# Performance work log

Hardware: AMD Instinct MI355X
Metric: run time of the kernel (lower is better)

## Reference

```python
import jax, jax.numpy as jnp
import numpy as np

H = 64      # num query heads
HKV = 8     # num key/value heads
D = 64      # head_dim
HID = 2880  # hidden_size
B = 8       # batch (num sequences)
Q = 16      # query tokens per sequence
P = 128     # kv pages per sequence
PAGE = 16   # kv page size
NPAGES = 2048  # total pages in cache pool
NEG = -1e9  # finite stand-in for -inf mask (avoids inf arithmetic; exp underflows to 0 identically)


def setup_inputs() -> dict:
    key = jax.random.key(0)
    ks = jax.random.split(key, 6)
    n = B * Q
    S = P * PAGE
    hidden_states = jax.random.normal(ks[0], (n, HID), jnp.float32) * 0.02
    kv_cache_at_layer = jax.random.normal(ks[1], (NPAGES, 2, PAGE, HKV, D), jnp.float32)
    qkv_dim = D * (H + 2 * HKV)
    w_qkv = jax.random.normal(ks[2], (qkv_dim, HID), jnp.float32) * 0.02
    b_qkv = jnp.zeros((qkv_dim,), jnp.float32)
    w_o = jax.random.normal(ks[3], (HID, H * D), jnp.float32) * 0.02
    b_o = jnp.zeros((HID,), jnp.float32)
    sinks = jax.random.normal(ks[4], (H,), jnp.float32)
    qo_indptr = (jnp.arange(B + 1) * Q).astype(jnp.int32)
    kv_page_indptr = (jnp.arange(B + 1) * P).astype(jnp.int32)
    kv_last_page_lens = jnp.full((B,), PAGE, jnp.int32)
    kv_page_indices = jnp.asarray(np.random.default_rng(0).permutation(NPAGES)[:B * P], jnp.int32)
    # causal mask: query i of each sequence sits at absolute position S - Q + i
    qpos = S - Q + jnp.arange(Q)
    mask = jnp.where(jnp.arange(S)[None, :] <= qpos[:, None], 0.0, NEG).astype(jnp.float32)
    attention_mask = jnp.broadcast_to(mask[None], (B, Q, S)).reshape(-1)
    return dict(hidden_states=hidden_states, kv_cache_at_layer=kv_cache_at_layer,
                attention_mask=attention_mask, w_qkv=w_qkv, b_qkv=b_qkv, w_o=w_o, b_o=b_o,
                sinks=sinks, qo_indptr=qo_indptr, kv_page_indptr=kv_page_indptr,
                kv_last_page_lens=kv_last_page_lens, kv_page_indices=kv_page_indices)


def reference(hidden_states, kv_cache_at_layer, attention_mask, w_qkv, b_qkv, w_o, b_o,
              sinks, qo_indptr, kv_page_indptr, kv_last_page_lens, kv_page_indices):
    n = hidden_states.shape[0]
    b = qo_indptr.shape[0] - 1
    q_len = n // b                              # uniform ragged layout (see setup)
    p = kv_page_indices.shape[0] // b
    page = kv_cache_at_layer.shape[2]
    s = p * page
    g = H // HKV                                # query heads per kv head (GQA groups)
    scaling = D ** -0.5

    qkv = hidden_states @ w_qkv.T + b_qkv                       # [n, (H+2*HKV)*D]
    q = qkv[:, :H * D].reshape(b, q_len, HKV, g, D) * scaling    # [b q hkv g d]

    pages = kv_page_indices.reshape(b, p)
    k = kv_cache_at_layer[pages, 0].reshape(b, s, HKV, D)        # gather pages -> [b s hkv d]
    v = kv_cache_at_layer[pages, 1].reshape(b, s, HKV, D)

    scores = jnp.einsum('bqhgd,bshd->bhgqs', q, k).astype(jnp.float32)
    mask = attention_mask.reshape(b, q_len, s)
    # keys beyond the valid portion of the last page are invalid
    valid = jnp.arange(s)[None, :] < ((p - 1) * page + kv_last_page_lens[:, None])
    mask = jnp.where(valid[:, None, :], mask, NEG)
    scores = scores + mask[:, None, None, :, :]

    # online-softmax merge across pages is equivalent to this single pass;
    # running max starts at 0 in the original, hence the clamp to 0
    m = jnp.maximum(scores.max(axis=-1), 0.0)                    # [b hkv g q]
    pexp = jnp.exp(scores - m[..., None])                        # [b hkv g q s]
    sink = sinks.reshape(HKV, g).astype(jnp.float32)
    sum_exp = pexp.sum(axis=-1) + jnp.exp(sink[None, :, :, None] - m)
    num = jnp.einsum('bhgqs,bshd->bhgqd', pexp, v.astype(jnp.float32))
    attn = num / sum_exp[..., None]                              # [b hkv g q d]
    attn = attn.transpose(0, 3, 1, 2, 4).reshape(n, H * D)       # q (h d)
    return attn.astype(hidden_states.dtype) @ w_o.T + b_o
```

## Files before the change

### kernel.cpp

```cpp
#include <hip/hip_runtime.h>
#include <hip/hip_bf16.h>

#define BB      8
#define QL      16
#define NHKV    8
#define NG      8
#define DD      64
#define HIDN    2880
#define PP      128
#define PGSZ    16
#define SS      2048
#define NQ      4096
#define NSPLIT  8
#define KSQ     5
#define KCQ     576
#define KSO     8
#define KCO     512

typedef short bf16x8 __attribute__((ext_vector_type(8)));
typedef short short4v __attribute__((ext_vector_type(4)));
typedef float f32x4  __attribute__((ext_vector_type(4)));

__device__ inline short f2bf(float f) {
  __hip_bfloat16 h = __float2bfloat16(f);
  union { __hip_bfloat16 h; short s; } u; u.h = h;
  return u.s;
}

__device__ inline float bf2f(short s) {
  union { float f; unsigned u; } u;
  u.u = ((unsigned)(unsigned short)s) << 16;
  return u.f;
}

__device__ inline bf16x8 cvt8(float4 a, float4 b) {
  bf16x8 r;
  r[0] = f2bf(a.x); r[1] = f2bf(a.y); r[2] = f2bf(a.z); r[3] = f2bf(a.w);
  r[4] = f2bf(b.x); r[5] = f2bf(b.y); r[6] = f2bf(b.z); r[7] = f2bf(b.w);
  return r;
}

__device__ inline bf16x8 pack8(const float* __restrict__ p) {
  float4 a = *(const float4*)p;
  float4 b = *(const float4*)(p + 4);
  return cvt8(a, b);
}

__global__ __launch_bounds__(256) void k_qkv_split(const float* __restrict__ hid,
                                                   const float* __restrict__ wq,
                                                   short* __restrict__ qpart) {
  const int n0 = blockIdx.x * 32;
  const int ks = blockIdx.y;
  const int tid = threadIdx.x;
  const int wid = tid >> 6, lane = tid & 63;
  const int lo = lane & 15, hi = lane >> 4;
  const int m0 = wid * 32;

  const float* xr0 = hid + (size_t)(m0 + lo) * HIDN;
  const float* xr1 = hid + (size_t)(m0 + 16 + lo) * HIDN;
  const float* wr0 = wq + (size_t)(n0 + lo) * HIDN;
  const float* wr1 = wq + (size_t)(n0 + 16 + lo) * HIDN;
  const int kb = ks * KCQ + hi * 8;

  f32x4 acc[2][2];
#pragma unroll
  for (int mt = 0; mt < 2; ++mt)
#pragma unroll
    for (int nt = 0; nt < 2; ++nt) acc[mt][nt] = (f32x4){0.f, 0.f, 0.f, 0.f};

  float4 bufA[4][2], bufB[4][2];
#define LOADQ(dst, kk) { \
    dst[0][0] = *(const float4*)(xr0 + (kk)); dst[0][1] = *(const float4*)(xr0 + (kk) + 4); \
    dst[1][0] = *(const float4*)(xr1 + (kk)); dst[1][1] = *(const float4*)(xr1 + (kk) + 4); \
    dst[2][0] = *(const float4*)(wr0 + (kk)); dst[2][1] = *(const float4*)(wr0 + (kk) + 4); \
    dst[3][0] = *(const float4*)(wr1 + (kk)); dst[3][1] = *(const float4*)(wr1 + (kk) + 4); }
#define MFMAQ(buf) { \
    bf16x8 a0 = cvt8(buf[0][0], buf[0][1]); \
    bf16x8 a1 = cvt8(buf[1][0], buf[1][1]); \
    bf16x8 w0 = cvt8(buf[2][0], buf[2][1]); \
    bf16x8 w1 = cvt8(buf[3][0], buf[3][1]); \
    acc[0][0] = __builtin_amdgcn_mfma_f32_16x16x32_bf16(a0, w0, acc[0][0], 0, 0, 0); \
    acc[0][1] = __builtin_amdgcn_mfma_f32_16x16x32_bf16(a0, w1, acc[0][1], 0, 0, 0); \
    acc[1][0] = __builtin_amdgcn_mfma_f32_16x16x32_bf16(a1, w0, acc[1][0], 0, 0, 0); \
    acc[1][1] = __builtin_amdgcn_mfma_f32_16x16x32_bf16(a1, w1, acc[1][1], 0, 0, 0); }

  LOADQ(bufA, kb);
#pragma unroll
  for (int it = 0; it < 9; ++it) {
    const int kk = kb + it * 64;
    LOADQ(bufB, kk + 32);
    MFMAQ(bufA);
    if (it < 8) LOADQ(bufA, kk + 64);
    MFMAQ(bufB);
  }
#undef LOADQ
#undef MFMAQ

  short* qp = qpart + (size_t)ks * 128 * NQ;
#pragma unroll
  for (int mt = 0; mt < 2; ++mt)
#pragma unroll
    for (int nt = 0; nt < 2; ++nt)
#pragma unroll
      for (int r = 0; r < 4; ++r) {
        int m = m0 + mt * 16 + hi * 4 + r;
        int n = n0 + nt * 16 + lo;
        qp[(size_t)m * NQ + n] = f2bf(acc[mt][nt][r]);
      }
}

__global__ __launch_bounds__(256) void k_attn(const float* __restrict__ kvc,
                                              const int* __restrict__ pidx,
                                              const int* __restrict__ llen,
                                              const short* __restrict__ qpart,
                                              const float* __restrict__ bq,
                                              short* __restrict__ opart,
                                              float* __restrict__ lbuf) {
  const int blk = blockIdx.x;
  const int pair = blk >> 3, split = blk & 7;
  const int b = pair >> 3, kvh = pair & 7;
  const int tid = threadIdx.x;
  const int wid = tid >> 6, lane = tid & 63;
  const int lo = lane & 15, hi = lane >> 4;
  const int wrow = wid * 32;

  __shared__ short plds[128][72];
  __shared__ float vlds[64][65];

  bf16x8 qf[2][2];
#pragma unroll
  for (int mt = 0; mt < 2; ++mt) {
    int r = wrow + mt * 16 + lo;
    int g = r >> 4, qq = r & 15;
    int m = b * QL + qq;
    int h = kvh * NG + g;
#pragma unroll
    for (int kg = 0; kg < 2; ++kg) {
      int n = h * DD + kg * 32 + hi * 8;
      float4 bb0 = *(const float4*)(bq + n);
      float4 bb1 = *(const float4*)(bq + n + 4);
      float s[8];
      s[0] = bb0.x; s[1] = bb0.y; s[2] = bb0.z; s[3] = bb0.w;
      s[4] = bb1.x; s[5] = bb1.y; s[6] = bb1.z; s[7] = bb1.w;
#pragma unroll
      for (int k2 = 0; k2 < KSQ; ++k2) {
        bf16x8 p = *(const bf16x8*)(qpart + ((size_t)k2 * 128 + m) * NQ + n);
#pragma unroll
        for (int j = 0; j < 8; ++j) s[j] += bf2f(p[j]);
      }
      bf16x8 q8;
#pragma unroll
      for (int j = 0; j < 8; ++j) q8[j] = f2bf(s[j] * 0.125f);
      qf[mt][kg] = q8;
    }
  }

  float l_part[2][4];
  f32x4 o_acc[2][4];
#pragma unroll
  for (int mt = 0; mt < 2; ++mt)
#pragma unroll
    for (int j = 0; j < 4; ++j) l_part[mt][j] = 0.f;
#pragma unroll
  for (int mt = 0; mt < 2; ++mt)
#pragma unroll
    for (int dt = 0; dt < 4; ++dt) o_acc[mt][dt] = (f32x4){0.f, 0.f, 0.f, 0.f};

  const int sKeepEnd = (PP - 1) * PGSZ + llen[b];
  const int* pib = pidx + b * PP;
  const int sBeg = split * (SS / NSPLIT);
  const int sEnd = sBeg + (SS / NSPLIT);

  for (int s0 = sBeg; s0 < sEnd; s0 += 64) {
    const int p0 = s0 >> 4;

    float4 vreg[4];
    const int vsr = tid >> 4;
    const int vc4 = (tid & 15) * 4;
#pragma unroll
    for (int pc = 0; pc < 4; ++pc) {
      int pg = pib[p0 + pc];
      vreg[pc] = *(const float4*)(kvc +
          ((((size_t)pg * 2 + 1) * PGSZ + vsr) * NHKV + kvh) * DD + vc4);
    }

    f32x4 sc[2][4];
#pragma unroll
    for (int mt = 0; mt < 2; ++mt)
#pragma unroll
      for (int nt = 0; nt < 4; ++nt) sc[mt][nt] = (f32x4){0.f, 0.f, 0.f, 0.f};

#pragma unroll
    for (int nt = 0; nt < 4; ++nt) {
      int pg = pib[p0 + nt];
      const float* kp = kvc + ((((size_t)pg * 2 + 0) * PGSZ + lo) * NHKV + kvh) * DD;
#pragma unroll
      for (int kg = 0; kg < 2; ++kg) {
        bf16x8 kf = pack8(kp + kg * 32 + hi * 8);
        sc[0][nt] = __builtin_amdgcn_mfma_f32_16x16x32_bf16(qf[0][kg], kf, sc[0][nt], 0, 0, 0);
        sc[1][nt] = __builtin_amdgcn_mfma_f32_16x16x32_bf16(qf[1][kg], kf, sc[1][nt], 0, 0, 0);
      }
    }

    if (s0 + 64 > SS - QL) {
#pragma unroll
      for (int mt = 0; mt < 2; ++mt)
#pragma unroll
        for (int j = 0; j < 4; ++j) {
          int r = wrow + mt * 16 + hi * 4 + j;
          int qq = r & 15;
          int sLimQ = (SS - QL) + qq;
#pragma unroll
          for (int nt = 0; nt < 4; ++nt) {
            int s = s0 + nt * 16 + lo;
            bool keep = (s <= sLimQ) && (s < sKeepEnd);
            sc[mt][nt][j] = keep ? sc[mt][nt][j] : -1.0e9f;
          }
        }
    }

#pragma unroll
    for (int mt = 0; mt < 2; ++mt)
#pragma unroll
      for (int j = 0; j < 4; ++j)
#pragma unroll
        for (int nt = 0; nt < 4; ++nt) {
          float p = __expf(sc[mt][nt][j]);
          sc[mt][nt][j] = p;
          l_part[mt][j] += p;
        }

    __syncthreads();
#pragma unroll
    for (int pc = 0; pc < 4; ++pc) {
      int sl = pc * 16 + vsr;
      vlds[sl][vc4]     = vreg[pc].x;
      vlds[sl][vc4 + 1] = vreg[pc].y;
      vlds[sl][vc4 + 2] = vreg[pc].z;
      vlds[sl][vc4 + 3] = vreg[pc].w;
    }
#pragma unroll
    for (int mt = 0; mt < 2; ++mt)
#pragma unroll
      for (int j = 0; j < 4; ++j) {
        int r = wrow + mt * 16 + hi * 4 + j;
#pragma unroll
        for (int nt = 0; nt < 4; ++nt)
          plds[r][nt * 16 + lo] = f2bf(sc[mt][nt][j]);
      }
    __syncthreads();

#pragma unroll
    for (int kg = 0; kg < 2; ++kg) {
      bf16x8 pa[2];
      pa[0] = *(const bf16x8*)(&plds[wrow + lo][kg * 32 + hi * 8]);
      pa[1] = *(const bf16x8*)(&plds[wrow + 16 + lo][kg * 32 + hi * 8]);
#pragma unroll
      for (int dt = 0; dt < 4; ++dt) {
        bf16x8 vf;
#pragma unroll
        for (int j = 0; j < 8; ++j)
          vf[j] = f2bf(vlds[kg * 32 + hi * 8 + j][dt * 16 + lo]);
        o_acc[0][dt] = __builtin_amdgcn_mfma_f32_16x16x32_bf16(pa[0], vf, o_acc[0][dt], 0, 0, 0);
        o_acc[1][dt] = __builtin_amdgcn_mfma_f32_16x16x32_bf16(pa[1], vf, o_acc[1][dt], 0, 0, 0);
      }
    }
  }

#pragma unroll
  for (int mt = 0; mt < 2; ++mt)
#pragma unroll
    for (int j = 0; j < 4; ++j)
#pragma unroll
      for (int off = 1; off < 16; off <<= 1)
        l_part[mt][j] += __shfl_xor(l_part[mt][j], off, 64);

  short* op = opart + (size_t)(pair * NSPLIT + split) * 128 * DD;
#pragma unroll
  for (int mt = 0; mt < 2; ++mt)
#pragma unroll
    for (int dt = 0; dt < 4; ++dt)
#pragma unroll
      for (int j = 0; j < 4; ++j) {
        int r = wrow + mt * 16 + hi * 4 + j;
        op[r * DD + dt * 16 + lo] = f2bf(o_acc[mt][dt][j]);
      }
  if (lo == 0) {
#pragma unroll
    for (int mt = 0; mt < 2; ++mt)
#pragma unroll
      for (int j = 0; j < 4; ++j) {
        int r = wrow + mt * 16 + hi * 4 + j;
        lbuf[(size_t)(pair * NSPLIT + split) * 128 + r] = l_part[mt][j];
      }
  }
}

__global__ __launch_bounds__(256) void k_merge(const short* __restrict__ opart,
                                               const float* __restrict__ lbuf,
                                               const float* __restrict__ sinks,
                                               short* __restrict__ attnbf) {
  const int pair = blockIdx.x;
  const int b = pair >> 3, kvh = pair & 7;
  const int tid = threadIdx.x;

  __shared__ float Ls[128];
  if (tid < 128) {
    int r = tid, g = r >> 4;
    float L = __expf(sinks[kvh * NG + g]);
#pragma unroll
    for (int s2 = 0; s2 < NSPLIT; ++s2)
      L += lbuf[(size_t)(pair * NSPLIT + s2) * 128 + r];
    Ls[r] = L;
  }
  __syncthreads();

  for (int u = tid; u < 128 * 16; u += 256) {
    int r = u >> 4, c4 = (u & 15) * 4;
    float o0 = 0.f, o1 = 0.f, o2 = 0.f, o3 = 0.f;
#pragma unroll
    for (int s2 = 0; s2 < NSPLIT; ++s2) {
      short4v pv = *(const short4v*)(opart +
          ((size_t)(pair * NSPLIT + s2) * 128 + r) * DD + c4);
      o0 += bf2f(pv[0]); o1 += bf2f(pv[1]); o2 += bf2f(pv[2]); o3 += bf2f(pv[3]);
    }
    float inv = 1.0f / Ls[r];
    int g = r >> 4, qq = r & 15;
    int h = kvh * NG + g;
    short4v ov;
    ov[0] = f2bf(o0 * inv); ov[1] = f2bf(o1 * inv);
    ov[2] = f2bf(o2 * inv); ov[3] = f2bf(o3 * inv);
    *(short4v*)(attnbf + (size_t)(b * QL + qq) * NQ + h * DD + c4) = ov;
  }
}

__global__ __launch_bounds__(256) void k_out_split(const short* __restrict__ attnbf,
                                                   const float* __restrict__ wo,
                                                   short* __restrict__ outpart) {
  const int n0 = blockIdx.x * 32;
  const int ks = blockIdx.y;
  const int tid = threadIdx.x;
  const int wid = tid >> 6, lane = tid & 63;
  const int lo = lane & 15, hi = lane >> 4;
  const int m0 = wid * 32;

  const short* ar0 = attnbf + (size_t)(m0 + lo) * NQ;
  const short* ar1 = attnbf + (size_t)(m0 + 16 + lo) * NQ;
  const float* wr0 = wo + (size_t)(n0 + lo) * NQ;
  const float* wr1 = wo + (size_t)(n0 + 16 + lo) * NQ;
  const int kb = ks * KCO + hi * 8;

  f32x4 acc[2][2];
#pragma unroll
  for (int mt = 0; mt < 2; ++mt)
#pragma unroll
    for (int nt = 0; nt < 2; ++nt) acc[mt][nt] = (f32x4){0.f, 0.f, 0.f, 0.f};

  bf16x8 aA[2], aB[2];
  float4 wA[2][2], wB[2][2];
#define LOADO(adst, wdst, kk) { \
    adst[0] = *(const bf16x8*)(ar0 + (kk)); \
    adst[1] = *(const bf16x8*)(ar1 + (kk)); \
    wdst[0][0] = *(const float4*)(wr0 + (kk)); wdst[0][1] = *(const float4*)(wr0 + (kk) + 4); \
    wdst[1][0] = *(const float4*)(wr1 + (kk)); wdst[1][1] = *(const float4*)(wr1 + (kk) + 4); }
#define MFMAO(abuf, wbuf) { \
    bf16x8 ww0 = cvt8(wbuf[0][0], wbuf[0][1]); \
    bf16x8 ww1 = cvt8(wbuf[1][0], wbuf[1][1]); \
    acc[0][0] = __builtin_amdgcn_mfma_f32_16x16x32_bf16(abuf[0], ww0, acc[0][0], 0, 0, 0); \
    acc[0][1] = __builtin_amdgcn_mfma_f32_16x16x32_bf16(abuf[0], ww1, acc[0][1], 0, 0, 0); \
    acc[1][0] = __builtin_amdgcn_mfma_f32_16x16x32_bf16(abuf[1], ww0, acc[1][0], 0, 0, 0); \
    acc[1][1] = __builtin_amdgcn_mfma_f32_16x16x32_bf16(abuf[1], ww1, acc[1][1], 0, 0, 0); }

  LOADO(aA, wA, kb);
#pragma unroll
  for (int it = 0; it < 8; ++it) {
    const int kk = kb + it * 64;
    LOADO(aB, wB, kk + 32);
    MFMAO(aA, wA);
    if (it < 7) LOADO(aA, wA, kk + 64);
    MFMAO(aB, wB);
  }
#undef LOADO
#undef MFMAO

  short* op = outpart + (size_t)ks * 128 * HIDN;
#pragma unroll
  for (int mt = 0; mt < 2; ++mt)
#pragma unroll
    for (int nt = 0; nt < 2; ++nt)
#pragma unroll
      for (int r = 0; r < 4; ++r) {
        int m = m0 + mt * 16 + hi * 4 + r;
        int n = n0 + nt * 16 + lo;
        op[(size_t)m * HIDN + n] = f2bf(acc[mt][nt][r]);
      }
}

__global__ __launch_bounds__(256) void k_ored(const short* __restrict__ outpart,
                                              const float* __restrict__ bo,
                                              float* __restrict__ out) {
  int idx = blockIdx.x * 256 + threadIdx.x;
  int m = idx / 720;
  int n = (idx - m * 720) * 4;
  float4 v = *(const float4*)(bo + n);
#pragma unroll
  for (int ks = 0; ks < KSO; ++ks) {
    short4v p = *(const short4v*)(outpart + ((size_t)ks * 128 + m) * HIDN + n);
    v.x += bf2f(p[0]); v.y += bf2f(p[1]); v.z += bf2f(p[2]); v.w += bf2f(p[3]);
  }
  *(float4*)(out + (size_t)m * HIDN + n) = v;
}

extern "C" void kernel_launch(void* const* d_in, const int* in_sizes, int n_in,
                              void* d_out, int out_size, void* d_ws, size_t ws_size,
                              hipStream_t stream) {
  const float* hid   = (const float*)d_in[0];
  const float* kvc   = (const float*)d_in[1];
  const float* wq    = (const float*)d_in[3];
  const float* bq    = (const float*)d_in[4];
  const float* wo    = (const float*)d_in[5];
  const float* bo    = (const float*)d_in[6];
  const float* sinks = (const float*)d_in[7];
  const int* llen    = (const int*)d_in[10];
  const int* pidx    = (const int*)d_in[11];
  float* out = (float*)d_out;

  char* ws = (char*)d_ws;
  short* qpart   = (short*)(ws + 0);
  short* attnbf  = (short*)(ws + 5242880);
  short* opart   = (short*)(ws + 6291456);
  float* lbuf    = (float*)(ws + 14680064);
  short* outpart = (short*)(ws + 14942208);

  k_qkv_split<<<dim3(128, KSQ), dim3(256), 0, stream>>>(hid, wq, qpart);
  k_attn<<<dim3(BB * NHKV * NSPLIT), dim3(256), 0, stream>>>(kvc, pidx, llen, qpart, bq, opart, lbuf);
  k_merge<<<dim3(BB * NHKV), dim3(256), 0, stream>>>(opart, lbuf, sinks, attnbf);
  k_out_split<<<dim3(HIDN / 32, KSO), dim3(256), 0, stream>>>(attnbf, wo, outpart);
  k_ored<<<dim3(360), dim3(256), 0, stream>>>(outpart, bo, out);
}
```

Before: 128.7 us.

## Replace split-K output partials and reduce kernel with fp32 atomics; widen merge grid

The output projection now accumulates each K-split's fp32 result directly into the output with atomicAdd, adding the bias on split 0. This removes the bf16 partial buffer write and the separate reduction kernel, at the cost of a memset and contended atomics. The merge kernel is also split four ways across the head dimension to launch more blocks. The atomic summation order is nondeterministic, and the partials are no longer rounded to bf16 before being summed.

```diff
diff --git a/kernel.cpp b/kernel.cpp
--- a/kernel.cpp
+++ b/kernel.cpp
@@ -300,7 +300,7 @@
                                                const float* __restrict__ lbuf,
                                                const float* __restrict__ sinks,
                                                short* __restrict__ attnbf) {
-  const int pair = blockIdx.x;
+  const int pair = blockIdx.x >> 2, quarter = blockIdx.x & 3;
   const int b = pair >> 3, kvh = pair & 7;
   const int tid = threadIdx.x;
 
@@ -315,8 +315,8 @@
   }
   __syncthreads();
 
-  for (int u = tid; u < 128 * 16; u += 256) {
-    int r = u >> 4, c4 = (u & 15) * 4;
+  for (int u = tid; u < 128 * 4; u += 256) {
+    int r = u >> 2, c4 = (quarter * 4 + (u & 3)) * 4;
     float o0 = 0.f, o1 = 0.f, o2 = 0.f, o3 = 0.f;
 #pragma unroll
     for (int s2 = 0; s2 < NSPLIT; ++s2) {
@@ -334,9 +334,10 @@
   }
 }
 
-__global__ __launch_bounds__(256) void k_out_split(const short* __restrict__ attnbf,
-                                                   const float* __restrict__ wo,
-                                                   short* __restrict__ outpart) {
+__global__ __launch_bounds__(256) void k_out_atomic(const short* __restrict__ attnbf,
+                                                    const float* __restrict__ wo,
+                                                    const float* __restrict__ bo,
+                                                    float* __restrict__ out) {
   const int n0 = blockIdx.x * 32;
   const int ks = blockIdx.y;
   const int tid = threadIdx.x;
@@ -383,7 +384,6 @@
 #undef LOADO
 #undef MFMAO
 
-  short* op = outpart + (size_t)ks * 128 * HIDN;
 #pragma unroll
   for (int mt = 0; mt < 2; ++mt)
 #pragma unroll
@@ -392,23 +392,10 @@
       for (int r = 0; r < 4; ++r) {
         int m = m0 + mt * 16 + hi * 4 + r;
         int n = n0 + nt * 16 + lo;
-        op[(size_t)m * HIDN + n] = f2bf(acc[mt][nt][r]);
-      }
-}
-
-__global__ __launch_bounds__(256) void k_ored(const short* __restrict__ outpart,
-                                              const float* __restrict__ bo,
-                                              float* __restrict__ out) {
-  int idx = blockIdx.x * 256 + threadIdx.x;
-  int m = idx / 720;
-  int n = (idx - m * 720) * 4;
-  float4 v = *(const float4*)(bo + n);
-#pragma unroll
-  for (int ks = 0; ks < KSO; ++ks) {
-    short4v p = *(const short4v*)(outpart + ((size_t)ks * 128 + m) * HIDN + n);
-    v.x += bf2f(p[0]); v.y += bf2f(p[1]); v.z += bf2f(p[2]); v.w += bf2f(p[3]);
-  }
-  *(float4*)(out + (size_t)m * HIDN + n) = v;
+        float v = acc[mt][nt][r];
+        if (ks == 0) v += bo[n];
+        atomicAdd(&out[(size_t)m * HIDN + n], v);
+      }
 }
 
 extern "C" void kernel_launch(void* const* d_in, const int* in_sizes, int n_in,
@@ -426,15 +413,14 @@
   float* out = (float*)d_out;
 
   char* ws = (char*)d_ws;
-  short* qpart   = (short*)(ws + 0);
-  short* attnbf  = (short*)(ws + 5242880);
-  short* opart   = (short*)(ws + 6291456);
-  float* lbuf    = (float*)(ws + 14680064);
-  short* outpart = (short*)(ws + 14942208);
-
+  short* qpart  = (short*)(ws + 0);
+  short* opart  = (short*)(ws + 5242880);
+  float* lbuf   = (float*)(ws + 13631488);
+  short* attnbf = (short*)(ws + 13893632);
+
+  hipMemsetAsync(out, 0, (size_t)128 * HIDN * sizeof(float), stream);
   k_qkv_split<<<dim3(128, KSQ), dim3(256), 0, stream>>>(hid, wq, qpart);
   k_attn<<<dim3(BB * NHKV * NSPLIT), dim3(256), 0, stream>>>(kvc, pidx, llen, qpart, bq, opart, lbuf);
-  k_merge<<<dim3(BB * NHKV), dim3(256), 0, stream>>>(opart, lbuf, sinks, attnbf);
-  k_out_split<<<dim3(HIDN / 32, KSO), dim3(256), 0, stream>>>(attnbf, wo, outpart);
-  k_ored<<<dim3(360), dim3(256), 0, stream>>>(outpart, bo, out);
-}
+  k_merge<<<dim3(BB * NHKV * 4), dim3(256), 0, stream>>>(opart, lbuf, sinks, attnbf);
+  k_out_atomic<<<dim3(HIDN / 32, KSO), dim3(256), 0, stream>>>(attnbf, wo, bo, out);
+}
```

Result: slower. 135.4 us (+5.2%).
